# Optimization experiments

Measured on AMD Instinct MI355X. Metric: run time of the kernel, lower is better.

The kernel has to match this reference:

```python
import jax, jax.numpy as jnp
import numpy as np

# ---- module config (init kwargs) ----
EMB = 256
HIDDEN = 256
L, H, P = 4, 8, 4
CH = HIDDEN // H
PADDING_MODE = "zeros"   # 'zeros' or 'border'
ALIGN_CORNERS = False
# feature pyramid level shapes (height, width), static
SHAPES = np.array([[128, 128], [64, 64], [32, 32], [16, 16]], dtype=np.int32)
LEVEL_STARTS = np.concatenate([[0], np.cumsum(SHAPES.prod(-1))[:-1]]).astype(np.int32)

B, N = 8, 1024
I = int(SHAPES.prod(-1).sum())  # 21760


def setup_inputs() -> dict:
    key = jax.random.key(0)
    ks = jax.random.split(key, 8)
    scale = 0.02
    return {
        "img": jax.random.normal(ks[0], (B, I, EMB), jnp.float32),
        "img_shapes": jnp.asarray(SHAPES),
        "queries": jax.random.normal(ks[1], (B, N, EMB), jnp.float32),
        "reference_points": jax.random.uniform(ks[2], (B, N, 2), dtype=jnp.float32),
        "W_img": jax.random.normal(ks[3], (EMB, HIDDEN), jnp.float32) * scale,
        "b_img": jnp.zeros((HIDDEN,), jnp.float32),
        "W_q": jax.random.normal(ks[4], (EMB, H * L * P * 3), jnp.float32) * scale,
        "b_q": jnp.zeros((H * L * P * 3,), jnp.float32),
        "W_out": jax.random.normal(ks[5], (HIDDEN, EMB), jnp.float32) * scale,
        "b_out": jnp.zeros((EMB,), jnp.float32),
    }


def _msda(img, points, attn):
    """Multiscale deformable attention core.
    img:    [B, I, H, CH] flattened pyramid features
    points: [B, N, H, L, P, 2] (x, y) in [0, 1]
    attn:   [B, N, H, L, P]
    returns [B, N, H, CH]
    """
    b, _, h_, ch = img.shape
    n = points.shape[1]
    img_t = img.transpose(0, 2, 1, 3)  # [B, H, I, CH]
    levels = []
    for l in range(L):
        hh, ww = int(SHAPES[l, 0]), int(SHAPES[l, 1])
        start = int(LEVEL_STARTS[l])
        p = points[:, :, :, l]  # [B, N, H, P, 2]
        # grid_sample pixel mapping (after the module's 2*p-1 normalization)
        if ALIGN_CORNERS:
            x = p[..., 0] * (ww - 1)
            y = p[..., 1] * (hh - 1)
        else:
            x = p[..., 0] * ww - 0.5
            y = p[..., 1] * hh - 0.5
        x0 = jnp.floor(x); y0 = jnp.floor(y)
        wx = x - x0;       wy = y - y0
        x0i = x0.astype(jnp.int32); y0i = y0.astype(jnp.int32)
        acc = jnp.zeros((b, h_, n * P, ch), img.dtype)
        corners = [
            (x0i,     y0i,     (1 - wx) * (1 - wy)),
            (x0i + 1, y0i,     wx * (1 - wy)),
            (x0i,     y0i + 1, (1 - wx) * wy),
            (x0i + 1, y0i + 1, wx * wy),
        ]
        for xi, yi, cw in corners:
            if PADDING_MODE == "zeros":
                valid = (xi >= 0) & (xi < ww) & (yi >= 0) & (yi < hh)
                cw = cw * valid.astype(cw.dtype)
            xc = jnp.clip(xi, 0, ww - 1)
            yc = jnp.clip(yi, 0, hh - 1)
            idx = start + yc * ww + xc                              # [B, N, H, P]
            idx_t = idx.transpose(0, 2, 1, 3).reshape(b, h_, n * P)  # [B, H, N*P]
            g = jnp.take_along_axis(img_t, idx_t[..., None], axis=2)  # [B, H, N*P, CH]
            cw_t = cw.transpose(0, 2, 1, 3).reshape(b, h_, n * P, 1)
            acc = acc + cw_t * g
        levels.append(acc.reshape(b, h_, n, P, ch))
    samples = jnp.stack(levels, axis=3)            # [B, H, N, L, P, CH]
    attn_t = attn.transpose(0, 2, 1, 3, 4)          # [B, H, N, L, P]
    return jnp.einsum("bhnlpc,bhnlp->bnhc", samples, attn_t)


def reference(img, img_shapes, queries, reference_points, W_img, b_img, W_q, b_q, W_out, b_out):
    b, i_, _ = img.shape
    n = queries.shape[1]
    qp = (queries @ W_q + b_q).reshape(b, n, H, L, P, 3)
    offsets = qp[..., :2]                            # [B, N, H, L, P, 2]
    attn = jax.nn.softmax(qp[..., 2].reshape(b, n, H, L * P), axis=-1).reshape(b, n, H, L, P)
    img_p = (img @ W_img + b_img).reshape(b, i_, H, CH)
    shapes_f = img_shapes.astype(jnp.float32)        # [L, 2] (h, w)
    # faithful to source: offsets / img_shapes[:, None, :]
    sampling_points = reference_points[:, :, None, None, None, :] + offsets / shapes_f[:, None, :]
    out = _msda(img_p, sampling_points, attn)        # [B, N, H, CH]
    return out.reshape(b, n, HIDDEN) @ W_out + b_out
```

## Files before the change

kernel.cpp:

```cpp
#include <hip/hip_runtime.h>
#include <type_traits>
#include <utility>

#define B_    8
#define NQ_   1024
#define I_    21760
#define EMB_  256
#define HID_  256
#define H_    8
#define CH_   32

typedef float  f32x4  __attribute__((ext_vector_type(4)));
typedef __bf16 bf16x8 __attribute__((ext_vector_type(8)));
typedef short  s16x8  __attribute__((ext_vector_type(8)));

template <typename V, typename = void>
struct bf16_mfma_native : std::false_type {};
template <typename V>
struct bf16_mfma_native<V, std::void_t<decltype(__builtin_amdgcn_mfma_f32_16x16x32_bf16(
    std::declval<V>(), std::declval<V>(), std::declval<f32x4>(), 0, 0, 0))>>
    : std::true_type {};

template <typename V>
__device__ __forceinline__ f32x4 mfma_dispatch(V a, V b, f32x4 c) {
  if constexpr (bf16_mfma_native<V>::value) {
    return __builtin_amdgcn_mfma_f32_16x16x32_bf16(a, b, c, 0, 0, 0);
  } else {
    return __builtin_amdgcn_mfma_f32_16x16x32_bf16(
        __builtin_bit_cast(s16x8, a), __builtin_bit_cast(s16x8, b), c, 0, 0, 0);
  }
}

__device__ __forceinline__ f32x4 MFMA(s16x8 a, s16x8 b, f32x4 c) {
  return mfma_dispatch(__builtin_bit_cast(bf16x8, a), __builtin_bit_cast(bf16x8, b), c);
}

__device__ __forceinline__ unsigned short f2bf(float f) {
  unsigned u = __float_as_uint(f);
  u += 0x7fffu + ((u >> 16) & 1u);
  return (unsigned short)(u >> 16);
}

template <int NS, int OUTM>
__global__ __launch_bounds__(512) void gemm_k256(
    const float* __restrict__ A, const float* __restrict__ W,
    const float* __restrict__ bias, void* __restrict__ Out,
    const int N, const int Mtiles) {
  __shared__ __align__(16) short lds[32 * 264];
  const int tid  = threadIdx.x;
  const int lane = tid & 63;
  const int wave = tid >> 6;
  const int quad = lane >> 4;
  const int ln   = lane & 15;

  s16x8 bfrag[NS][8];
  float bv[NS];
#pragma unroll
  for (int st = 0; st < NS; ++st) {
    const int ng = st * 128 + wave * 16 + ln;
    bv[st] = bias[ng];
#pragma unroll
    for (int ks = 0; ks < 8; ++ks) {
      s16x8 f;
#pragma unroll
      for (int j = 0; j < 8; ++j)
        f[j] = (short)f2bf(W[(ks * 32 + quad * 8 + j) * N + ng]);
      bfrag[st][ks] = f;
    }
  }

  const int sr = tid >> 4;
  const int sc = (tid & 15) * 16;

  int t = blockIdx.x;
  float4 v0, v1, v2, v3;
  if (t < Mtiles) {
    const float4* src = (const float4*)(A + ((size_t)t * 32 + sr) * 256 + sc);
    v0 = src[0]; v1 = src[1]; v2 = src[2]; v3 = src[3];
  }

  for (; t < Mtiles; t += gridDim.x) {
    {
      s16x8 p0, p1;
      p0[0] = (short)f2bf(v0.x); p0[1] = (short)f2bf(v0.y);
      p0[2] = (short)f2bf(v0.z); p0[3] = (short)f2bf(v0.w);
      p0[4] = (short)f2bf(v1.x); p0[5] = (short)f2bf(v1.y);
      p0[6] = (short)f2bf(v1.z); p0[7] = (short)f2bf(v1.w);
      p1[0] = (short)f2bf(v2.x); p1[1] = (short)f2bf(v2.y);
      p1[2] = (short)f2bf(v2.z); p1[3] = (short)f2bf(v2.w);
      p1[4] = (short)f2bf(v3.x); p1[5] = (short)f2bf(v3.y);
      p1[6] = (short)f2bf(v3.z); p1[7] = (short)f2bf(v3.w);
      *(s16x8*)&lds[sr * 264 + sc]     = p0;
      *(s16x8*)&lds[sr * 264 + sc + 8] = p1;
    }
    __syncthreads();

    {
      const int tn = t + gridDim.x;
      if (tn < Mtiles) {
        const float4* src = (const float4*)(A + ((size_t)tn * 32 + sr) * 256 + sc);
        v0 = src[0]; v1 = src[1]; v2 = src[2]; v3 = src[3];
      }
    }

    f32x4 acc[NS][2];
#pragma unroll
    for (int st = 0; st < NS; ++st) {
      acc[st][0] = f32x4{bv[st], bv[st], bv[st], bv[st]};
      acc[st][1] = acc[st][0];
    }
#pragma unroll
    for (int ks = 0; ks < 8; ++ks) {
      s16x8 a0 = *(const s16x8*)&lds[ln * 264 + ks * 32 + quad * 8];
      s16x8 a1 = *(const s16x8*)&lds[(ln + 16) * 264 + ks * 32 + quad * 8];
#pragma unroll
      for (int st = 0; st < NS; ++st) {
        acc[st][0] = MFMA(a0, bfrag[st][ks], acc[st][0]);
        acc[st][1] = MFMA(a1, bfrag[st][ks], acc[st][1]);
      }
    }
    const size_t rowBase = (size_t)t * 32;
    if constexpr (OUTM == 1) {
      const int tb  = (int)(rowBase / I_);
      const int ir0 = (int)(rowBase - (size_t)tb * I_);
      unsigned short* O = (unsigned short*)Out;
#pragma unroll
      for (int st = 0; st < NS; ++st) {
        const int ng = st * 128 + wave * 16 + ln;
        const int hh = ng >> 5, cc = ng & 31;
        const size_t pl = (size_t)(tb * 8 + hh) * I_;
#pragma unroll
        for (int rt = 0; rt < 2; ++rt) {
#pragma unroll
          for (int r = 0; r < 4; ++r) {
            const size_t i = pl + (size_t)(ir0 + rt * 16 + quad * 4 + r);
            O[i * 32 + cc] = f2bf(acc[st][rt][r]);
          }
        }
      }
    } else {
      float* O = (float*)Out;
#pragma unroll
      for (int st = 0; st < NS; ++st) {
        const int ng = st * 128 + wave * 16 + ln;
#pragma unroll
        for (int rt = 0; rt < 2; ++rt) {
#pragma unroll
          for (int r = 0; r < 4; ++r) {
            const size_t m = rowBase + rt * 16 + quad * 4 + r;
            O[m * N + ng] = acc[st][rt][r];
          }
        }
      }
    }
    __syncthreads();
  }
}

__global__ __launch_bounds__(128) void msda_fused_kernel(
    const unsigned int* __restrict__ imgp,
    const float* __restrict__ qp, const float* __restrict__ refp,
    float* __restrict__ out) {
  __shared__ __align__(16) float sw[128][4];
  __shared__ __align__(16) int   sib[128][2];
  const int bid = ((blockIdx.x & 7) << 10) | (blockIdx.x >> 3);
  const int b   = bid >> 10;
  const int tid = threadIdx.x;

  {
    const int h = tid >> 4, lp = tid & 15, l = lp >> 2;
    const int ww = 128 >> l;
    const int start = (65536 - (65536 >> (2 * l))) / 3;
    const float invsh = __uint_as_float((unsigned)(120 + l) << 23);

    const float* qb = qp + (size_t)bid * 384 + h * 48 + lp * 3;
    const float ox = qb[0], oy = qb[1], z = qb[2];
    float m = z;
    m = fmaxf(m, __shfl_xor(m, 1, 16));
    m = fmaxf(m, __shfl_xor(m, 2, 16));
    m = fmaxf(m, __shfl_xor(m, 4, 16));
    m = fmaxf(m, __shfl_xor(m, 8, 16));
    float e = __expf(z - m);
    float s = e;
    s += __shfl_xor(s, 1, 16);
    s += __shfl_xor(s, 2, 16);
    s += __shfl_xor(s, 4, 16);
    s += __shfl_xor(s, 8, 16);
    const float a = e / s;

    const float rx = refp[bid * 2], ry = refp[bid * 2 + 1];
    const float x = (rx + ox * invsh) * (float)ww - 0.5f;
    const float y = (ry + oy * invsh) * (float)ww - 0.5f;
    const float x0f = floorf(x), y0f = floorf(y);
    const float wx = x - x0f, wy = y - y0f;
    const int x0 = (int)x0f, y0 = (int)y0f;

    const int xb = min(max(x0, 0), ww - 2);
    float u0 = 0.f, u1 = 0.f;
    if (x0 >= 0 && x0 < ww)         { if (x0 == xb)     u0 += 1.f - wx; else u1 += 1.f - wx; }
    if (x0 + 1 >= 0 && x0 + 1 < ww) { if (x0 + 1 == xb) u0 += wx;       else u1 += wx; }
    const float wy0 = (y0 >= 0     && y0 < ww)     ? a * (1.f - wy) : 0.f;
    const float wy1 = (y0 + 1 >= 0 && y0 + 1 < ww) ? a * wy         : 0.f;
    const int yc0 = min(max(y0, 0), ww - 1);
    const int yc1 = min(max(y0 + 1, 0), ww - 1);

    const int pb = (b * 8 + h) * I_ + start + xb;
    sw[tid][0] = wy0 * u0; sw[tid][1] = wy0 * u1;
    sw[tid][2] = wy1 * u0; sw[tid][3] = wy1 * u1;
    sib[tid][0] = (pb + yc0 * ww) * 16;
    sib[tid][1] = (pb + yc1 * ww) * 16;
  }
  __syncthreads();

  const int h = tid >> 4, c2 = tid & 15;
  const int p  = c2 >> 3;
  const int cp = ((c2 & 7) << 1) + (p << 4);
  float a0 = 0.f, a1 = 0.f, a2 = 0.f, a3 = 0.f;
#pragma unroll
  for (int lp = 0; lp < 16; ++lp) {
    const float4 w4 = *(const float4*)sw[h * 16 + lp];
    const int2   ib = *(const int2*)sib[h * 16 + lp];
    const float w0 = p ? w4.y : w4.x;
    const float w1 = p ? w4.w : w4.z;
    const uint2 ua = *(const uint2*)&imgp[ib.x + cp];
    const uint2 ub = *(const uint2*)&imgp[ib.y + cp];
    a0 += w0 * __uint_as_float(ua.x << 16);
    a1 += w0 * __uint_as_float(ua.x & 0xffff0000u);
    a2 += w0 * __uint_as_float(ua.y << 16);
    a3 += w0 * __uint_as_float(ua.y & 0xffff0000u);
    a0 += w1 * __uint_as_float(ub.x << 16);
    a1 += w1 * __uint_as_float(ub.x & 0xffff0000u);
    a2 += w1 * __uint_as_float(ub.y << 16);
    a3 += w1 * __uint_as_float(ub.y & 0xffff0000u);
  }
  a0 += __shfl_xor(a0, 8);
  a1 += __shfl_xor(a1, 8);
  a2 += __shfl_xor(a2, 8);
  a3 += __shfl_xor(a3, 8);
  float2 r;
  r.x = p ? a2 : a0;
  r.y = p ? a3 : a1;
  *(float2*)&out[(size_t)bid * 256 + h * 32 + ((c2 & 7) << 2) + (p << 1)] = r;
}

#define OFF_IMGP 0ULL
#define OFF_QP   89128960ULL
#define OFF_MSDA 101711872ULL
#define WS_NEEDED 110100480ULL

extern "C" void kernel_launch(void* const* d_in, const int* in_sizes, int n_in,
                              void* d_out, int out_size, void* d_ws, size_t ws_size,
                              hipStream_t stream) {
  const float* img     = (const float*)d_in[0];
  const float* queries = (const float*)d_in[2];
  const float* refp    = (const float*)d_in[3];
  const float* W_img   = (const float*)d_in[4];
  const float* b_img   = (const float*)d_in[5];
  const float* W_q     = (const float*)d_in[6];
  const float* b_q     = (const float*)d_in[7];
  const float* W_out   = (const float*)d_in[8];
  const float* b_out   = (const float*)d_in[9];

  if (ws_size < WS_NEEDED) return;

  char* ws = (char*)d_ws;
  unsigned short* imgp = (unsigned short*)(ws + OFF_IMGP);
  float* qp   = (float*)(ws + OFF_QP);
  float* msda = (float*)(ws + OFF_MSDA);

  hipLaunchKernelGGL((gemm_k256<2, 1>), dim3(512), dim3(512), 0, stream,
                     img, W_img, b_img, (void*)imgp, 256, I_ * B_ / 32);
  hipLaunchKernelGGL((gemm_k256<3, 0>), dim3(256), dim3(512), 0, stream,
                     queries, W_q, b_q, (void*)qp, 384, B_ * NQ_ / 32);
  hipLaunchKernelGGL(msda_fused_kernel, dim3(B_ * NQ_), dim3(128), 0, stream,
                     (const unsigned int*)imgp, qp, refp, msda);
  hipLaunchKernelGGL((gemm_k256<2, 0>), dim3(256), dim3(512), 0, stream,
                     msda, W_out, b_out, d_out, 256, B_ * NQ_ / 32);
}
```

Baseline: 339.7 us.

## Fuse all stages into one cooperative persistent kernel with grid syncs

Merges the image projection GEMM, query projection GEMM, MSDA sampling and output GEMM into a single cooperative kernel of 256 blocks of 512 threads, separated by grid-wide barriers. The MSDA phase now loops over 32 queries per block, four queries at a time, instead of one query per 128-thread block. The aim is to remove kernel launch gaps and tail effects between stages. The cost is fewer blocks for the large image GEMM (256 instead of 512), grid-sync overhead, and lower MSDA parallelism. A fallback path launches separate kernels if the cooperative launch fails.

```diff
diff --git a/kernel.cpp b/kernel.cpp
--- a/kernel.cpp
+++ b/kernel.cpp
@@ -1,4 +1,5 @@
 #include <hip/hip_runtime.h>
+#include <hip/hip_cooperative_groups.h>
 #include <type_traits>
 #include <utility>
 
@@ -42,11 +43,10 @@
 }
 
 template <int NS, int OUTM>
-__global__ __launch_bounds__(512) void gemm_k256(
+__device__ __forceinline__ void gemm_phase(
     const float* __restrict__ A, const float* __restrict__ W,
     const float* __restrict__ bias, void* __restrict__ Out,
-    const int N, const int Mtiles) {
-  __shared__ __align__(16) short lds[32 * 264];
+    const int N, const int Mtiles, short* __restrict__ lds) {
   const int tid  = threadIdx.x;
   const int lane = tid & 63;
   const int wave = tid >> 6;
@@ -157,90 +157,137 @@
   }
 }
 
-__global__ __launch_bounds__(128) void msda_fused_kernel(
+__device__ __forceinline__ void msda_phase(
     const unsigned int* __restrict__ imgp,
     const float* __restrict__ qp, const float* __restrict__ refp,
+    float* __restrict__ out, char* __restrict__ smem) {
+  float (*sw)[4]  = (float(*)[4])smem;
+  int   (*sib)[2] = (int(*)[2])(smem + 8192);
+  const int tid = threadIdx.x;
+  const int u = tid >> 7, t = tid & 127;
+  const int bk = blockIdx.x;
+
+  for (int it = 0; it < 8; ++it) {
+    const int bid = ((bk & 7) << 10) | ((bk >> 3) << 5) | (it << 2) | u;
+    const int b   = bid >> 10;
+    {
+      const int h = t >> 4, lp = t & 15, l = lp >> 2;
+      const int ww = 128 >> l;
+      const int start = (65536 - (65536 >> (2 * l))) / 3;
+      const float invsh = __uint_as_float((unsigned)(120 + l) << 23);
+
+      const float* qb = qp + (size_t)bid * 384 + h * 48 + lp * 3;
+      const float ox = qb[0], oy = qb[1], z = qb[2];
+      float m = z;
+      m = fmaxf(m, __shfl_xor(m, 1, 16));
+      m = fmaxf(m, __shfl_xor(m, 2, 16));
+      m = fmaxf(m, __shfl_xor(m, 4, 16));
+      m = fmaxf(m, __shfl_xor(m, 8, 16));
+      float e = __expf(z - m);
+      float s = e;
+      s += __shfl_xor(s, 1, 16);
+      s += __shfl_xor(s, 2, 16);
+      s += __shfl_xor(s, 4, 16);
+      s += __shfl_xor(s, 8, 16);
+      const float a = e / s;
+
+      const float rx = refp[bid * 2], ry = refp[bid * 2 + 1];
+      const float x = (rx + ox * invsh) * (float)ww - 0.5f;
+      const float y = (ry + oy * invsh) * (float)ww - 0.5f;
+      const float x0f = floorf(x), y0f = floorf(y);
+      const float wx = x - x0f, wy = y - y0f;
+      const int x0 = (int)x0f, y0 = (int)y0f;
+
+      const int xb = min(max(x0, 0), ww - 2);
+      float u0 = 0.f, u1 = 0.f;
+      if (x0 >= 0 && x0 < ww)         { if (x0 == xb)     u0 += 1.f - wx; else u1 += 1.f - wx; }
+      if (x0 + 1 >= 0 && x0 + 1 < ww) { if (x0 + 1 == xb) u0 += wx;       else u1 += wx; }
+      const float wy0 = (y0 >= 0     && y0 < ww)     ? a * (1.f - wy) : 0.f;
+      const float wy1 = (y0 + 1 >= 0 && y0 + 1 < ww) ? a * wy         : 0.f;
+      const int yc0 = min(max(y0, 0), ww - 1);
+      const int yc1 = min(max(y0 + 1, 0), ww - 1);
+
+      const int pb = (b * 8 + h) * I_ + start + xb;
+      sw[tid][0] = wy0 * u0; sw[tid][1] = wy0 * u1;
+      sw[tid][2] = wy1 * u0; sw[tid][3] = wy1 * u1;
+      sib[tid][0] = (pb + yc0 * ww) * 16;
+      sib[tid][1] = (pb + yc1 * ww) * 16;
+    }
+    __syncthreads();
+
+    {
+      const int h = t >> 4, c2 = t & 15;
+      const int p  = c2 >> 3;
+      const int cp = ((c2 & 7) << 1) + (p << 4);
+      float a0 = 0.f, a1 = 0.f, a2 = 0.f, a3 = 0.f;
+#pragma unroll
+      for (int lp = 0; lp < 16; ++lp) {
+        const float4 w4 = *(const float4*)sw[(u << 7) + h * 16 + lp];
+        const int2   ib = *(const int2*)sib[(u << 7) + h * 16 + lp];
+        const float w0 = p ? w4.y : w4.x;
+        const float w1 = p ? w4.w : w4.z;
+        const uint2 ua = *(const uint2*)&imgp[ib.x + cp];
+        const uint2 ub = *(const uint2*)&imgp[ib.y + cp];
+        a0 += w0 * __uint_as_float(ua.x << 16);
+        a1 += w0 * __uint_as_float(ua.x & 0xffff0000u);
+        a2 += w0 * __uint_as_float(ua.y << 16);
+        a3 += w0 * __uint_as_float(ua.y & 0xffff0000u);
+        a0 += w1 * __uint_as_float(ub.x << 16);
+        a1 += w1 * __uint_as_float(ub.x & 0xffff0000u);
+        a2 += w1 * __uint_as_float(ub.y << 16);
+        a3 += w1 * __uint_as_float(ub.y & 0xffff0000u);
+      }
+      a0 += __shfl_xor(a0, 8);
+      a1 += __shfl_xor(a1, 8);
+      a2 += __shfl_xor(a2, 8);
+      a3 += __shfl_xor(a3, 8);
+      float2 r;
+      r.x = p ? a2 : a0;
+      r.y = p ? a3 : a1;
+      *(float2*)&out[(size_t)bid * 256 + h * 32 + ((c2 & 7) << 2) + (p << 1)] = r;
+    }
+    __syncthreads();
+  }
+}
+
+__global__ __launch_bounds__(512, 2) void mega_kernel(
+    const float* __restrict__ img, const float* __restrict__ queries,
+    const float* __restrict__ refp, const float* __restrict__ W_img,
+    const float* __restrict__ b_img, const float* __restrict__ W_q,
+    const float* __restrict__ b_q, const float* __restrict__ W_out,
+    const float* __restrict__ b_out, unsigned short* __restrict__ imgp,
+    float* __restrict__ qp, float* __restrict__ msda,
     float* __restrict__ out) {
-  __shared__ __align__(16) float sw[128][4];
-  __shared__ __align__(16) int   sib[128][2];
-  const int bid = ((blockIdx.x & 7) << 10) | (blockIdx.x >> 3);
-  const int b   = bid >> 10;
-  const int tid = threadIdx.x;
-
-  {
-    const int h = tid >> 4, lp = tid & 15, l = lp >> 2;
-    const int ww = 128 >> l;
-    const int start = (65536 - (65536 >> (2 * l))) / 3;
-    const float invsh = __uint_as_float((unsigned)(120 + l) << 23);
-
-    const float* qb = qp + (size_t)bid * 384 + h * 48 + lp * 3;
-    const float ox = qb[0], oy = qb[1], z = qb[2];
-    float m = z;
-    m = fmaxf(m, __shfl_xor(m, 1, 16));
-    m = fmaxf(m, __shfl_xor(m, 2, 16));
-    m = fmaxf(m, __shfl_xor(m, 4, 16));
-    m = fmaxf(m, __shfl_xor(m, 8, 16));
-    float e = __expf(z - m);
-    float s = e;
-    s += __shfl_xor(s, 1, 16);
-    s += __shfl_xor(s, 2, 16);
-    s += __shfl_xor(s, 4, 16);
-    s += __shfl_xor(s, 8, 16);
-    const float a = e / s;
-
-    const float rx = refp[bid * 2], ry = refp[bid * 2 + 1];
-    const float x = (rx + ox * invsh) * (float)ww - 0.5f;
-    const float y = (ry + oy * invsh) * (float)ww - 0.5f;
-    const float x0f = floorf(x), y0f = floorf(y);
-    const float wx = x - x0f, wy = y - y0f;
-    const int x0 = (int)x0f, y0 = (int)y0f;
-
-    const int xb = min(max(x0, 0), ww - 2);
-    float u0 = 0.f, u1 = 0.f;
-    if (x0 >= 0 && x0 < ww)         { if (x0 == xb)     u0 += 1.f - wx; else u1 += 1.f - wx; }
-    if (x0 + 1 >= 0 && x0 + 1 < ww) { if (x0 + 1 == xb) u0 += wx;       else u1 += wx; }
-    const float wy0 = (y0 >= 0     && y0 < ww)     ? a * (1.f - wy) : 0.f;
-    const float wy1 = (y0 + 1 >= 0 && y0 + 1 < ww) ? a * wy         : 0.f;
-    const int yc0 = min(max(y0, 0), ww - 1);
-    const int yc1 = min(max(y0 + 1, 0), ww - 1);
-
-    const int pb = (b * 8 + h) * I_ + start + xb;
-    sw[tid][0] = wy0 * u0; sw[tid][1] = wy0 * u1;
-    sw[tid][2] = wy1 * u0; sw[tid][3] = wy1 * u1;
-    sib[tid][0] = (pb + yc0 * ww) * 16;
-    sib[tid][1] = (pb + yc1 * ww) * 16;
-  }
-  __syncthreads();
-
-  const int h = tid >> 4, c2 = tid & 15;
-  const int p  = c2 >> 3;
-  const int cp = ((c2 & 7) << 1) + (p << 4);
-  float a0 = 0.f, a1 = 0.f, a2 = 0.f, a3 = 0.f;
-#pragma unroll
-  for (int lp = 0; lp < 16; ++lp) {
-    const float4 w4 = *(const float4*)sw[h * 16 + lp];
-    const int2   ib = *(const int2*)sib[h * 16 + lp];
-    const float w0 = p ? w4.y : w4.x;
-    const float w1 = p ? w4.w : w4.z;
-    const uint2 ua = *(const uint2*)&imgp[ib.x + cp];
-    const uint2 ub = *(const uint2*)&imgp[ib.y + cp];
-    a0 += w0 * __uint_as_float(ua.x << 16);
-    a1 += w0 * __uint_as_float(ua.x & 0xffff0000u);
-    a2 += w0 * __uint_as_float(ua.y << 16);
-    a3 += w0 * __uint_as_float(ua.y & 0xffff0000u);
-    a0 += w1 * __uint_as_float(ub.x << 16);
-    a1 += w1 * __uint_as_float(ub.x & 0xffff0000u);
-    a2 += w1 * __uint_as_float(ub.y << 16);
-    a3 += w1 * __uint_as_float(ub.y & 0xffff0000u);
-  }
-  a0 += __shfl_xor(a0, 8);
-  a1 += __shfl_xor(a1, 8);
-  a2 += __shfl_xor(a2, 8);
-  a3 += __shfl_xor(a3, 8);
-  float2 r;
-  r.x = p ? a2 : a0;
-  r.y = p ? a3 : a1;
-  *(float2*)&out[(size_t)bid * 256 + h * 32 + ((c2 & 7) << 2) + (p << 1)] = r;
+  __shared__ __align__(16) char smem[32 * 264 * 2];
+
+  gemm_phase<2, 1>(img, W_img, b_img, (void*)imgp, 256, (B_ * I_) / 32, (short*)smem);
+  gemm_phase<3, 0>(queries, W_q, b_q, (void*)qp, 384, (B_ * NQ_) / 32, (short*)smem);
+
+  __threadfence();
+  cooperative_groups::this_grid().sync();
+
+  msda_phase((const unsigned int*)imgp, qp, refp, msda, smem);
+
+  __threadfence();
+  cooperative_groups::this_grid().sync();
+
+  gemm_phase<2, 0>(msda, W_out, b_out, (void*)out, 256, (B_ * NQ_) / 32, (short*)smem);
+}
+
+template <int NS, int OUTM>
+__global__ __launch_bounds__(512) void gemm_k256(
+    const float* __restrict__ A, const float* __restrict__ W,
+    const float* __restrict__ bias, void* __restrict__ Out,
+    const int N, const int Mtiles) {
+  __shared__ __align__(16) short lds[32 * 264];
+  gemm_phase<NS, OUTM>(A, W, bias, Out, N, Mtiles, lds);
+}
+
+__global__ __launch_bounds__(512) void msda_standalone(
+    const unsigned int* __restrict__ imgp, const float* __restrict__ qp,
+    const float* __restrict__ refp, float* __restrict__ out) {
+  __shared__ __align__(16) char smem[12288];
+  msda_phase(imgp, qp, refp, out, smem);
 }
 
 #define OFF_IMGP 0ULL
@@ -267,13 +314,24 @@
   unsigned short* imgp = (unsigned short*)(ws + OFF_IMGP);
   float* qp   = (float*)(ws + OFF_QP);
   float* msda = (float*)(ws + OFF_MSDA);
-
-  hipLaunchKernelGGL((gemm_k256<2, 1>), dim3(512), dim3(512), 0, stream,
-                     img, W_img, b_img, (void*)imgp, 256, I_ * B_ / 32);
-  hipLaunchKernelGGL((gemm_k256<3, 0>), dim3(256), dim3(512), 0, stream,
-                     queries, W_q, b_q, (void*)qp, 384, B_ * NQ_ / 32);
-  hipLaunchKernelGGL(msda_fused_kernel, dim3(B_ * NQ_), dim3(128), 0, stream,
-                     (const unsigned int*)imgp, qp, refp, msda);
-  hipLaunchKernelGGL((gemm_k256<2, 0>), dim3(256), dim3(512), 0, stream,
-                     msda, W_out, b_out, d_out, 256, B_ * NQ_ / 32);
-}
+  float* outf = (float*)d_out;
+
+  void* args[13] = {(void*)&img,  (void*)&queries, (void*)&refp,
+                    (void*)&W_img, (void*)&b_img,  (void*)&W_q,   (void*)&b_q,
+                    (void*)&W_out, (void*)&b_out,  (void*)&imgp,
+                    (void*)&qp,    (void*)&msda,   (void*)&outf};
+  hipError_t err = hipLaunchCooperativeKernel(
+      reinterpret_cast<void*>(mega_kernel), dim3(256), dim3(512), args, 0, stream);
+
+  if (err != hipSuccess) {
+    (void)hipGetLastError();
+    hipLaunchKernelGGL((gemm_k256<2, 1>), dim3(512), dim3(512), 0, stream,
+                       img, W_img, b_img, (void*)imgp, 256, I_ * B_ / 32);
+    hipLaunchKernelGGL((gemm_k256<3, 0>), dim3(256), dim3(512), 0, stream,
+                       queries, W_q, b_q, (void*)qp, 384, B_ * NQ_ / 32);
+    hipLaunchKernelGGL(msda_standalone, dim3(256), dim3(512), 0, stream,
+                       (const unsigned int*)imgp, qp, refp, msda);
+    hipLaunchKernelGGL((gemm_k256<2, 0>), dim3(256), dim3(512), 0, stream,
+                       msda, W_out, b_out, (void*)outf, 256, B_ * NQ_ / 32);
+  }
+}
```

After: 483.6 us. +42.3%, slower.

## Remap MSDA blocks to eight queries of one (batch, head) plane

Applied to the files above, without the earlier changes.

Each MSDA block used to handle one query across all 8 heads. It now handles 8 queries that share one (batch, head) pair, and the block index is swizzled so consecutive blocks map to different heads. All gathers in a block then hit a single head's feature plane, which should improve L2 locality for the bilinear sampling. The two projection GEMM launches also swap order, and output writes per block become 8 strided 128-byte segments rather than one contiguous row.

```diff
diff --git a/kernel.cpp b/kernel.cpp
--- a/kernel.cpp
+++ b/kernel.cpp
@@ -157,22 +157,29 @@
   }
 }
 
-__global__ __launch_bounds__(128) void msda_fused_kernel(
+__global__ __launch_bounds__(128) void msda_kernel(
     const unsigned int* __restrict__ imgp,
     const float* __restrict__ qp, const float* __restrict__ refp,
     float* __restrict__ out) {
   __shared__ __align__(16) float sw[128][4];
   __shared__ __align__(16) int   sib[128][2];
-  const int bid = ((blockIdx.x & 7) << 10) | (blockIdx.x >> 3);
-  const int b   = bid >> 10;
+  const int blk = blockIdx.x;
+  const int x   = blk & 7;
+  const int j   = blk >> 3;
+  const int c   = ((j >> 7) << 3) | x;
+  const int b   = c >> 3, h = c & 7;
+  const int qg  = j & 127;
   const int tid = threadIdx.x;
+  const int pl  = (b * 8 + h) * I_;
 
   {
-    const int h = tid >> 4, lp = tid & 15, l = lp >> 2;
+    const int q8 = tid >> 4, lp = tid & 15, l = lp >> 2;
     const int ww = 128 >> l;
     const int start = (65536 - (65536 >> (2 * l))) / 3;
     const float invsh = __uint_as_float((unsigned)(120 + l) << 23);
 
+    const int n   = (qg << 3) | q8;
+    const int bid = (b << 10) | n;
     const float* qb = qp + (size_t)bid * 384 + h * 48 + lp * 3;
     const float ox = qb[0], oy = qb[1], z = qb[2];
     float m = z;
@@ -189,10 +196,10 @@
     const float a = e / s;
 
     const float rx = refp[bid * 2], ry = refp[bid * 2 + 1];
-    const float x = (rx + ox * invsh) * (float)ww - 0.5f;
-    const float y = (ry + oy * invsh) * (float)ww - 0.5f;
-    const float x0f = floorf(x), y0f = floorf(y);
-    const float wx = x - x0f, wy = y - y0f;
+    const float px = (rx + ox * invsh) * (float)ww - 0.5f;
+    const float py = (ry + oy * invsh) * (float)ww - 0.5f;
+    const float x0f = floorf(px), y0f = floorf(py);
+    const float wx = px - x0f, wy = py - y0f;
     const int x0 = (int)x0f, y0 = (int)y0f;
 
     const int xb = min(max(x0, 0), ww - 2);
@@ -204,7 +211,7 @@
     const int yc0 = min(max(y0, 0), ww - 1);
     const int yc1 = min(max(y0 + 1, 0), ww - 1);
 
-    const int pb = (b * 8 + h) * I_ + start + xb;
+    const int pb = pl + start + xb;
     sw[tid][0] = wy0 * u0; sw[tid][1] = wy0 * u1;
     sw[tid][2] = wy1 * u0; sw[tid][3] = wy1 * u1;
     sib[tid][0] = (pb + yc0 * ww) * 16;
@@ -212,14 +219,14 @@
   }
   __syncthreads();
 
-  const int h = tid >> 4, c2 = tid & 15;
+  const int q8 = tid >> 4, c2 = tid & 15;
   const int p  = c2 >> 3;
   const int cp = ((c2 & 7) << 1) + (p << 4);
   float a0 = 0.f, a1 = 0.f, a2 = 0.f, a3 = 0.f;
 #pragma unroll
   for (int lp = 0; lp < 16; ++lp) {
-    const float4 w4 = *(const float4*)sw[h * 16 + lp];
-    const int2   ib = *(const int2*)sib[h * 16 + lp];
+    const float4 w4 = *(const float4*)sw[q8 * 16 + lp];
+    const int2   ib = *(const int2*)sib[q8 * 16 + lp];
     const float w0 = p ? w4.y : w4.x;
     const float w1 = p ? w4.w : w4.z;
     const uint2 ua = *(const uint2*)&imgp[ib.x + cp];
@@ -240,6 +247,7 @@
   float2 r;
   r.x = p ? a2 : a0;
   r.y = p ? a3 : a1;
+  const int bid = (b << 10) | (qg << 3) | q8;
   *(float2*)&out[(size_t)bid * 256 + h * 32 + ((c2 & 7) << 2) + (p << 1)] = r;
 }
 
@@ -268,11 +276,11 @@
   float* qp   = (float*)(ws + OFF_QP);
   float* msda = (float*)(ws + OFF_MSDA);
 
+  hipLaunchKernelGGL((gemm_k256<3, 0>), dim3(256), dim3(512), 0, stream,
+                     queries, W_q, b_q, (void*)qp, 384, B_ * NQ_ / 32);
   hipLaunchKernelGGL((gemm_k256<2, 1>), dim3(512), dim3(512), 0, stream,
                      img, W_img, b_img, (void*)imgp, 256, I_ * B_ / 32);
-  hipLaunchKernelGGL((gemm_k256<3, 0>), dim3(256), dim3(512), 0, stream,
-                     queries, W_q, b_q, (void*)qp, 384, B_ * NQ_ / 32);
-  hipLaunchKernelGGL(msda_fused_kernel, dim3(B_ * NQ_), dim3(128), 0, stream,
+  hipLaunchKernelGGL(msda_kernel, dim3(B_ * NQ_ * H_ / 8), dim3(128), 0, stream,
                      (const unsigned int*)imgp, qp, refp, msda);
   hipLaunchKernelGGL((gemm_k256<2, 0>), dim3(256), dim3(512), 0, stream,
                      msda, W_out, b_out, d_out, 256, B_ * NQ_ / 32);
```

New measurement: 338.2 us. No clear change (-0.5%).
